# Kernel tuning notes

Measured on AMD Instinct MI355X. Metric: run time of the kernel, lower is better.

The kernel has to match this reference:

```python
import jax, jax.numpy as jnp
import numpy as np

B, W, F = 16, 8192, 256

def setup_inputs() -> dict:
    key = jax.random.key(0)
    k1, k2 = jax.random.split(key)
    x = jax.random.normal(k1, (B, 1, W, F), dtype=jnp.float32)
    weights0 = jax.random.normal(k2, (F,), dtype=jnp.float32)
    return {"x": x, "weights0": weights0}

def reference(x, weights0):
    # x: [B, 1, W, F]; weights0: [F]
    w = jax.nn.sigmoid(weights0)                      # [F], constrained to (0,1)
    # The diag-matrix conv2d is mathematically an elementwise blend of adjacent
    # width positions: inter[i] = w * x[i] + (1-w) * x[i+1]
    inter = w * x[:, :, :-1, :] + (1.0 - w) * x[:, :, 1:, :]   # [B,1,W-1,F]
    b, one, width, f = x.shape
    out = jnp.zeros((b, one, 2 * width - 1, f), dtype=x.dtype)
    out = out.at[:, :, 0::2, :].set(x)                # even rows: originals
    out = out.at[:, :, 1::2, :].set(inter)            # odd rows: interpolated
    return out
```

## Files before the change

kernel.cpp:

```cpp
#include <hip/hip_runtime.h>
#include <math.h>

constexpr int B  = 16;
constexpr int W  = 8192;
constexpr int F  = 256;
constexpr int F4 = F / 4;
constexpr int OW = 2 * W - 1;

constexpr int TOTAL_F4 = B * OW * F4;
constexpr int BLOCK    = 256;
constexpr int GRID     = TOTAL_F4 / BLOCK;

__global__ __launch_bounds__(BLOCK) void upsampler_kernel(
    const float4* __restrict__ x4,
    const float*  __restrict__ w0,
    float4* __restrict__ out4)
{
    const unsigned tid  = blockIdx.x * BLOCK + threadIdx.x;
    const unsigned lane = tid & 63u;
    const unsigned rg   = tid >> 6;
    const unsigned b    = rg / (unsigned)OW;
    const unsigned row  = rg - b * (unsigned)OW;

    const float4* xb = x4 + (size_t)b * W * F4;

    float4 v;
    if ((row & 1u) == 0u) {
        v = xb[(size_t)(row >> 1) * F4 + lane];
    } else {
        const unsigned i = row >> 1;
        const float4 a = xb[(size_t)i       * F4 + lane];
        const float4 c = xb[(size_t)(i + 1) * F4 + lane];
        const float4 wv = ((const float4*)w0)[lane];
        float4 s;
        s.x = 1.0f / (1.0f + expf(-wv.x));
        s.y = 1.0f / (1.0f + expf(-wv.y));
        s.z = 1.0f / (1.0f + expf(-wv.z));
        s.w = 1.0f / (1.0f + expf(-wv.w));
        v.x = s.x * a.x + (1.0f - s.x) * c.x;
        v.y = s.y * a.y + (1.0f - s.y) * c.y;
        v.z = s.z * a.z + (1.0f - s.z) * c.z;
        v.w = s.w * a.w + (1.0f - s.w) * c.w;
    }
    out4[tid] = v;
}

extern "C" void kernel_launch(void* const* d_in, const int* in_sizes, int n_in,
                              void* d_out, int out_size, void* d_ws, size_t ws_size,
                              hipStream_t stream) {
    const float* x  = (const float*)d_in[0];
    const float* w0 = (const float*)d_in[1];
    float* out = (float*)d_out;

    upsampler_kernel<<<GRID, BLOCK, 0, stream>>>(
        (const float4*)x, w0, (float4*)out);
}
```

Measured before the change: 344.6 us.

## Map one thread per input row, writing both original and interpolated outputs

Remaps threads from one per output row to one per input row. Each thread loads x[p] once, writes it to the even output row, and writes the blend with x[p+1] to the odd row. This removes the integer division by OW and the separate reload of x[p] that even rows did before. It also switches to a fast exp2/rcp sigmoid and nontemporal stores to avoid polluting the cache. The risks are slightly lower sigmoid accuracy and fewer threads each doing two stores.

```diff
diff --git a/kernel.cpp b/kernel.cpp
--- a/kernel.cpp
+++ b/kernel.cpp
@@ -7,42 +7,50 @@
 constexpr int F4 = F / 4;
 constexpr int OW = 2 * W - 1;
 
-constexpr int TOTAL_F4 = B * OW * F4;
-constexpr int BLOCK    = 256;
-constexpr int GRID     = TOTAL_F4 / BLOCK;
+constexpr int THREADS = B * W * F4;
+constexpr int BLOCK   = 256;
+constexpr int GRID    = THREADS / BLOCK;
+
+typedef float f32x4 __attribute__((ext_vector_type(4)));
+
+__device__ __forceinline__ float fast_sigmoid(float w) {
+    const float e = __builtin_amdgcn_exp2f(w * -1.4426950408889634f);
+    return __builtin_amdgcn_rcpf(1.0f + e);
+}
 
 __global__ __launch_bounds__(BLOCK) void upsampler_kernel(
-    const float4* __restrict__ x4,
-    const float*  __restrict__ w0,
-    float4* __restrict__ out4)
+    const f32x4* __restrict__ x4,
+    const float* __restrict__ w0,
+    f32x4* __restrict__ out4)
 {
     const unsigned tid  = blockIdx.x * BLOCK + threadIdx.x;
     const unsigned lane = tid & 63u;
-    const unsigned rg   = tid >> 6;
-    const unsigned b    = rg / (unsigned)OW;
-    const unsigned row  = rg - b * (unsigned)OW;
+    const unsigned rw   = tid >> 6;
+    const unsigned b    = rw >> 13;
+    const unsigned p    = rw & (unsigned)(W - 1);
 
-    const float4* xb = x4 + (size_t)b * W * F4;
+    const f32x4* xb = x4   + (size_t)b * W  * F4;
+    f32x4*       ob = out4 + (size_t)b * OW * F4;
 
-    float4 v;
-    if ((row & 1u) == 0u) {
-        v = xb[(size_t)(row >> 1) * F4 + lane];
+    const f32x4 a = xb[(size_t)p * F4 + lane];
+
+    if (p < (unsigned)(W - 1)) {
+        const f32x4 c  = xb[(size_t)(p + 1) * F4 + lane];
+        const f32x4 wv = ((const f32x4*)w0)[lane];
+
+        f32x4 s;
+        s[0] = fast_sigmoid(wv[0]);
+        s[1] = fast_sigmoid(wv[1]);
+        s[2] = fast_sigmoid(wv[2]);
+        s[3] = fast_sigmoid(wv[3]);
+
+        const f32x4 v = s * a + (1.0f - s) * c;
+
+        __builtin_nontemporal_store(a, &ob[(size_t)p * (2 * F4) + lane]);
+        __builtin_nontemporal_store(v, &ob[(size_t)p * (2 * F4) + F4 + lane]);
     } else {
-        const unsigned i = row >> 1;
-        const float4 a = xb[(size_t)i       * F4 + lane];
-        const float4 c = xb[(size_t)(i + 1) * F4 + lane];
-        const float4 wv = ((const float4*)w0)[lane];
-        float4 s;
-        s.x = 1.0f / (1.0f + expf(-wv.x));
-        s.y = 1.0f / (1.0f + expf(-wv.y));
-        s.z = 1.0f / (1.0f + expf(-wv.z));
-        s.w = 1.0f / (1.0f + expf(-wv.w));
-        v.x = s.x * a.x + (1.0f - s.x) * c.x;
-        v.y = s.y * a.y + (1.0f - s.y) * c.y;
-        v.z = s.z * a.z + (1.0f - s.z) * c.z;
-        v.w = s.w * a.w + (1.0f - s.w) * c.w;
+        __builtin_nontemporal_store(a, &ob[(size_t)p * (2 * F4) + lane]);
     }
-    out4[tid] = v;
 }
 
 extern "C" void kernel_launch(void* const* d_in, const int* in_sizes, int n_in,
@@ -53,5 +61,5 @@
     float* out = (float*)d_out;
 
     upsampler_kernel<<<GRID, BLOCK, 0, stream>>>(
-        (const float4*)x, w0, (float4*)out);
+        (const f32x4*)x, w0, (f32x4*)out);
 }
```

Measured after the change: 349.4 us. About the same (+1.4%).
